# Performance work log

Hardware: AMD Instinct MI355X
Metric: run time of the kernel (lower is better)

## Reference

```python
import jax, jax.numpy as jnp
import numpy as np

N, C, T, V = 16, 64, 300, 25
NH, DK, DV = 4, 64, 64
DKH = DK // NH
DVH = DV // NH
EPS = 1e-5


def rel_to_abs(x):
    # x: (B, Nh, L, 2L-1) relative logits -> (B, Nh, L, L) absolute, via skew trick
    B, Nh, L, _ = x.shape
    x = jnp.pad(x, ((0, 0), (0, 0), (0, 0), (0, 1)))          # (B,Nh,L,2L)
    flat = x.reshape(B, Nh, L * 2 * L)
    flat = jnp.pad(flat, ((0, 0), (0, 0), (0, L - 1)))
    final = flat.reshape(B, Nh, L + 1, 2 * L - 1)
    return final[:, :, :L, L - 1:]


def setup_inputs() -> dict:
    key = jax.random.key(0)
    ks = jax.random.split(key, 12)
    return {
        "x": jax.random.normal(ks[0], (N, C, T, V), jnp.float32),
        "dbn_g": jax.random.normal(ks[1], (C * V,), jnp.float32),
        "dbn_b": jax.random.normal(ks[2], (C * V,), jnp.float32),
        "dbn_m": jax.random.normal(ks[3], (C * V,), jnp.float32) * 0.1,
        "dbn_v": jax.random.uniform(ks[4], (C * V,), jnp.float32, 0.5, 1.5),
        "qkv_w": jax.random.normal(ks[5], (2 * DK + DV, C), jnp.float32) * 0.05,
        "qkv_b": jax.random.normal(ks[6], (2 * DK + DV,), jnp.float32) * 0.05,
        "key_rel": jax.random.normal(ks[7], (2 * T - 1, DKH), jnp.float32),
        "attn_w": jax.random.normal(ks[8], (DV, DV), jnp.float32) * 0.05,
        "attn_b": jax.random.normal(ks[9], (DV,), jnp.float32) * 0.05,
        "bn_g": jax.random.normal(ks[10], (DV,), jnp.float32),
        "bn_b": jax.random.normal(ks[11], (DV,), jnp.float32),
        "bn_m": jnp.zeros((DV,), jnp.float32),
        "bn_v": jnp.ones((DV,), jnp.float32),
    }


def reference(x, dbn_g, dbn_b, dbn_m, dbn_v, qkv_w, qkv_b, key_rel,
              attn_w, attn_b, bn_g, bn_b, bn_m, bn_v):
    x_sum = x  # (N,C,T,V)
    # data_bn: BatchNorm1d (eval) over C*V channels on (N, C*V, T)
    xp = x.transpose(0, 1, 3, 2).reshape(N, C * V, T)
    xp = (xp - dbn_m[None, :, None]) * jax.lax.rsqrt(dbn_v + EPS)[None, :, None] \
         * dbn_g[None, :, None] + dbn_b[None, :, None]
    xn = xp.reshape(N, C, V, T).transpose(0, 1, 3, 2)          # (N,C,T,V)
    # per-joint temporal sequences: (N*V, C, T)
    xa = xn.transpose(0, 3, 1, 2).reshape(N * V, C, T)
    # 1x1 qkv conv
    qkv = jnp.einsum('oc,bct->bot', qkv_w, xa) + qkv_b[None, :, None]
    B = N * V
    q = qkv[:, :DK].reshape(B, NH, DKH, T) * (DKH ** -0.5)
    k = qkv[:, DK:2 * DK].reshape(B, NH, DKH, T)
    v = qkv[:, 2 * DK:].reshape(B, NH, DVH, T)
    logits = jnp.einsum('bhdt,bhds->bhts', q, k)               # (B,NH,T,T)
    rel = jnp.einsum('bhdt,md->bhtm', q, key_rel)              # (B,NH,T,2T-1)
    logits = logits + rel_to_abs(rel)
    w = jax.nn.softmax(logits, axis=-1)
    attn = jnp.einsum('bhts,bhds->bhtd', w, v)                 # (B,NH,T,DVH)
    attn = attn.transpose(0, 1, 3, 2).reshape(B, DV, T)        # combine heads
    attn = jnp.einsum('od,bdt->bot', attn_w, attn) + attn_b[None, :, None]
    out = attn.reshape(N, V, DV, T).transpose(0, 2, 3, 1)      # (N,DV,T,V)
    res = out + x_sum                                          # skip (down is None)
    res = (res - bn_m[None, :, None, None]) * jax.lax.rsqrt(bn_v + EPS)[None, :, None, None] \
          * bn_g[None, :, None, None] + bn_b[None, :, None, None]
    return jax.nn.relu(res)
```

## Files before the change

kernel.cpp:

```cpp
#include <hip/hip_runtime.h>
#include <hip/hip_bf16.h>
#include <cstddef>

#define NN 16
#define CC 64
#define TT 300
#define VV 25
#define NHH 4
#define DKHH 16
#define BB (NN * VV)
#define EPS 1e-5f
#define LOG2E 1.4426950408889634f

#define WS_QK    0
#define WS_V     7680000
#define WS_AH    11571200
#define WS_REL   15462400
#define WS_AWF   15472896
#define WS_AOFF  15474944
#define WS_SCO   15475008
#define WS_WFRAG 15475072
#define WS_QB2   15481216
#define WS_SCSH  15481408

typedef __attribute__((ext_vector_type(8))) short short8;
typedef __attribute__((ext_vector_type(4))) float float4v;

union U8 { short8 v; unsigned int w[4]; };

__device__ __forceinline__ unsigned int pk2(float a, float b) {
#if __has_builtin(__builtin_amdgcn_cvt_pk_bf16_f32)
    typedef __attribute__((ext_vector_type(2))) __bf16 bf2;
    union { bf2 v; unsigned u; } c;
    c.v = __builtin_amdgcn_cvt_pk_bf16_f32(a, b);
    return c.u;
#else
    union { float f; unsigned u; } x, y;
    x.f = a; y.f = b;
    unsigned ua = x.u + 0x7FFFu + ((x.u >> 16) & 1u);
    unsigned ub = y.u + 0x7FFFu + ((y.u >> 16) & 1u);
    return (ua >> 16) | (ub & 0xFFFF0000u);
#endif
}

__device__ __forceinline__ float ex2(float x) {
#if __has_builtin(__builtin_amdgcn_exp2f)
    return __builtin_amdgcn_exp2f(x);
#else
    return exp2f(x);
#endif
}

__device__ __forceinline__ float rcpf_(float x) {
#if __has_builtin(__builtin_amdgcn_rcpf)
    return __builtin_amdgcn_rcpf(x);
#else
    return 1.f / x;
#endif
}

__global__ __launch_bounds__(256) void k_pre(
    const float* __restrict__ dbn_g, const float* __restrict__ dbn_b,
    const float* __restrict__ dbn_m, const float* __restrict__ dbn_v,
    const float* __restrict__ qkv_w, const float* __restrict__ qkv_b,
    const float* __restrict__ key_rel,
    const float* __restrict__ attn_w, const float* __restrict__ attn_b,
    const float* __restrict__ bn_g, const float* __restrict__ bn_b,
    const float* __restrict__ bn_m, const float* __restrict__ bn_v,
    unsigned* __restrict__ W)
{
    const int jid = blockIdx.x * 256 + threadIdx.x;
    if (jid < 2624) {
        const int k = jid >> 6, lane = jid & 63, col = lane & 15, quad = lane >> 4;
        const int mt = k - 1, m = mt * 16 + col;
        const bool ok = (quad < 2) && (mt >= 0) && (m < 2 * TT - 1);
        unsigned w[4];
        #pragma unroll
        for (int j2 = 0; j2 < 4; ++j2) {
            const int c = quad * 8 + 2 * j2;
            const float v0 = ok ? key_rel[m * 16 + c] : 0.f;
            const float v1 = ok ? key_rel[m * 16 + c + 1] : 0.f;
            w[j2] = pk2(v0, v1);
        }
        *(uint4*)&W[WS_REL + k * 256 + lane * 4] = make_uint4(w[0], w[1], w[2], w[3]);
    } else if (jid < 3136) {
        const int e = jid - 2624;
        const int ot = e >> 7, ch = (e >> 6) & 1, lane = e & 63;
        const int col = lane & 15, quad = lane >> 4;
        const int o = ot * 16 + col;
        const float sc = bn_g[o] * rsqrtf(bn_v[o] + EPS);
        unsigned w[4];
        #pragma unroll
        for (int j2 = 0; j2 < 4; ++j2) {
            const int c = ch * 32 + quad * 8 + 2 * j2;
            w[j2] = pk2(attn_w[o * 64 + c] * sc, attn_w[o * 64 + c + 1] * sc);
        }
        *(uint4*)&W[WS_AWF + (ot * 2 + ch) * 256 + lane * 4] = make_uint4(w[0], w[1], w[2], w[3]);
    } else if (jid < 3200) {
        const int o = jid - 3136;
        const float sc = bn_g[o] * rsqrtf(bn_v[o] + EPS);
        ((float*)(W + WS_AOFF))[o] = attn_b[o] * sc + bn_b[o] - bn_m[o] * sc;
    } else if (jid < 3264) {
        const int o = jid - 3200;
        ((float*)(W + WS_SCO))[o] = bn_g[o] * rsqrtf(bn_v[o] + EPS);
    } else if (jid < 4800) {
        const int e = jid - 3264;
        const int ot = e >> 7, ch = (e >> 6) & 1, lane = e & 63;
        const int col = lane & 15, quad = lane >> 4;
        const int o = ot * 16 + col;
        const float qs = (o < 64) ? 0.25f * LOG2E : 1.f;
        unsigned w[4];
        #pragma unroll
        for (int j2 = 0; j2 < 4; ++j2) {
            const int c = ch * 32 + quad * 8 + 2 * j2;
            w[j2] = pk2(qkv_w[o * 64 + c] * qs, qkv_w[o * 64 + c + 1] * qs);
        }
        *(uint4*)&W[WS_WFRAG + (ot * 2 + ch) * 256 + lane * 4] = make_uint4(w[0], w[1], w[2], w[3]);
    } else if (jid < 4992) {
        const int o = jid - 4800;
        ((float*)(W + WS_QB2))[o] = qkv_b[o] * ((o < 64) ? 0.25f * LOG2E : 1.f);
    } else if (jid < 6592) {
        const int e = jid - 4992;
        const float sc = dbn_g[e] * rsqrtf(dbn_v[e] + EPS);
        const float sh = dbn_b[e] - dbn_m[e] * sc;
        ((float2*)(W + WS_SCSH))[e] = make_float2(sc, sh);
    }
}

__global__ __launch_bounds__(512) void k_qkv(
        const float* __restrict__ x, unsigned* __restrict__ W)
{
    const int tt = blockIdx.x, n = blockIdx.y, t0 = tt * 16;
    const int tid = threadIdx.x;
    const unsigned* wfrag = W + WS_WFRAG;
    const float* qb2 = (const float*)(W + WS_QB2);
    unsigned* qk_p = W + WS_QK;
    unsigned* v_p  = W + WS_V;

    __shared__ unsigned afrag[25 * 516];
    __shared__ float2 sls[1600];

    for (int i = tid; i < 1600; i += 512)
        sls[i] = ((const float2*)(W + WS_SCSH))[i];
    __syncthreads();

    for (int i = tid; i < 3200; i += 512) {
        const int f4 = i % 100, cp = i / 100;
        const int c0 = cp * 2;
        float4 xa = make_float4(0.f, 0.f, 0.f, 0.f);
        float4 xb = make_float4(0.f, 0.f, 0.f, 0.f);
        if (tt < 18 || f4 < 75) {
            const float* p = x + (size_t)(n * 64 + c0) * 7500 + tt * 400 + f4 * 4;
            xa = *(const float4*)p;
            xb = *(const float4*)(p + 7500);
        }
        const int ch = cp >> 4, qd = (cp >> 2) & 3, j2 = cp & 3;
        const float ea[4] = {xa.x, xa.y, xa.z, xa.w};
        const float eb[4] = {xb.x, xb.y, xb.z, xb.w};
        #pragma unroll
        for (int e = 0; e < 4; ++e) {
            const int flat = f4 * 4 + e;
            const int tl = (flat * 5243) >> 17;
            const int v  = flat - 25 * tl;
            const float2 s0 = sls[c0 * 25 + v];
            const float2 s1 = sls[c0 * 25 + 25 + v];
            const float a0 = fmaf(ea[e], s0.x, s0.y);
            const float a1 = fmaf(eb[e], s1.x, s1.y);
            afrag[v * 516 + (ch * 64 + qd * 16 + tl) * 4 + j2] = pk2(a0, a1);
        }
    }
    __syncthreads();

    const int wvv = tid >> 6, lane = tid & 63, col = lane & 15, quad = lane >> 4;
    const int otg = wvv >> 1, vh = wvv & 1;
    const int vlo = 13 * vh, vhi = vh ? 25 : 13;
    const float4v zero4 = {0.f, 0.f, 0.f, 0.f};
    const bool tvalid = (t0 + 4 * quad + 3 < TT);

    U8 bf[3][2]; float qb_l[3];
    #pragma unroll
    for (int i = 0; i < 3; ++i) {
        const int ot = 3 * otg + i;
        #pragma unroll
        for (int ch = 0; ch < 2; ++ch) {
            const uint4 u = *(const uint4*)&wfrag[(ot * 2 + ch) * 256 + lane * 4];
            bf[i][ch].w[0] = u.x; bf[i][ch].w[1] = u.y; bf[i][ch].w[2] = u.z; bf[i][ch].w[3] = u.w;
        }
        qb_l[i] = qb2[ot * 16 + col];
    }

    for (int v = vlo; v < vhi; ++v) {
        const int b = n * 25 + v;
        U8 a0, a1;
        { const uint4 u = *(const uint4*)&afrag[v * 516 + lane * 4];
          a0.w[0] = u.x; a0.w[1] = u.y; a0.w[2] = u.z; a0.w[3] = u.w; }
        { const uint4 u = *(const uint4*)&afrag[v * 516 + 256 + lane * 4];
          a1.w[0] = u.x; a1.w[1] = u.y; a1.w[2] = u.z; a1.w[3] = u.w; }
        #pragma unroll
        for (int i = 0; i < 3; ++i) {
            const int ot = 3 * otg + i;
            float4v acc = __builtin_amdgcn_mfma_f32_16x16x32_bf16(a0.v, bf[i][0].v, zero4, 0, 0, 0);
            acc = __builtin_amdgcn_mfma_f32_16x16x32_bf16(a1.v, bf[i][1].v, acc, 0, 0, 0);
            float val[4];
            #pragma unroll
            for (int r = 0; r < 4; ++r) val[r] = acc[r] + qb_l[i];
            if (ot < 8) {
                unsigned pk[4];
                #pragma unroll
                for (int r = 0; r < 4; ++r) {
                    const float p = __shfl_xor(val[r], 1);
                    pk[r] = pk2(val[r], p);
                }
                if (((col & 1) == 0) && tvalid) {
                    const int op = ot * 8 + (col >> 1);
                    *(uint4*)&qk_p[(size_t)(b * 64 + op) * TT + t0 + 4 * quad] =
                        make_uint4(pk[0], pk[1], pk[2], pk[3]);
                }
            } else {
                const int d = (ot - 8) * 16 + col;
                uint2 u;
                if (tvalid) { u.x = pk2(val[0], val[1]); u.y = pk2(val[2], val[3]); }
                else        { u.x = 0u; u.y = 0u; }
                *(uint2*)&v_p[(size_t)(b * 64 + d) * 152 + 8 * tt + 2 * quad] = u;
            }
        }
    }
}

__global__ __launch_bounds__(256, 4) void k_attn(unsigned* __restrict__ W)
{
    const int bh = blockIdx.x;
    const int half = blockIdx.y;
    const int b = bh >> 2, h = bh & 3;
    const int tid  = threadIdx.x;
    const int wave = tid >> 6, lane = tid & 63;
    const int col  = lane & 15, quad = lane >> 4;

    const unsigned* qk_p = W + WS_QK;
    const unsigned* v_p  = W + WS_V;
    unsigned* ah_p = W + WS_AH;
    const unsigned* relfrag = W + WS_REL;

    __shared__ unsigned kbuf[19 * 32 * 4];
    __shared__ unsigned vbuf[10 * 64 * 4];
    __shared__ float relbuf[4][16 * 68];

    for (int p = tid; p < 2432; p += 256) {
        const int c = p & 15, j2 = (p >> 4) & 3, qh = (p >> 6) & 1, st = p >> 7;
        kbuf[(st * 32 + qh * 16 + c) * 4 + j2] =
            qk_p[(size_t)(b * 64 + 32 + h * 8 + qh * 4 + j2) * TT + st * 16 + c];
    }
    for (int p = tid; p < 640; p += 256) {
        const int tq = p % 40, d = p / 40;
        const int off = (tq * 4 <= 148) ? tq * 4 : 144;
        const uint4 u = *(const uint4*)&v_p[(size_t)(b * 64 + h * 16 + d) * 152 + off];
        const int c = tq >> 2;
        const int l0 = (tq & 3) * 4;
        const unsigned uu[4] = {u.x, u.y, u.z, u.w};
        #pragma unroll
        for (int j = 0; j < 4; ++j) {
            const int local = l0 + j;
            const int q  = (local < 8) ? (local >> 1) : ((local - 8) >> 1);
            const int j2 = (local < 8) ? (local & 1) : (2 + (local & 1));
            vbuf[(c * 64 + q * 16 + d) * 4 + j2] = uu[j];
        }
    }
    __syncthreads();

    float* relw = &relbuf[wave][0];
    const float4v zero4 = {0.f, 0.f, 0.f, 0.f};
    U8 onef;
    onef.w[0] = onef.w[1] = onef.w[2] = onef.w[3] = 0x3F803F80u;

    const int ttlo = half ? 10 : 0;
    const int tthi = half ? 19 : 10;

    for (int tt = ttlo + wave; tt < tthi; tt += 4) {
        const int t0 = tt * 16;

        U8 qf;
        if (quad < 2) {
            int t = t0 + col; if (t > TT - 1) t = TT - 1;
            const size_t rb = (size_t)(b * 64 + h * 8 + quad * 4) * TT + t;
            qf.w[0] = qk_p[rb];
            qf.w[1] = qk_p[rb + TT];
            qf.w[2] = qk_p[rb + 2 * TT];
            qf.w[3] = qk_p[rb + 3 * TT];
        } else {
            qf.w[0] = qf.w[1] = qf.w[2] = qf.w[3] = 0u;
        }

        auto rel_ld = [&](int mt) -> uint4 {
            return *(const uint4*)&relfrag[(mt + 1) * 256 + lane * 4];
        };
        auto rel_do = [&](int mt, uint4 u) {
            U8 kr; kr.w[0] = u.x; kr.w[1] = u.y; kr.w[2] = u.z; kr.w[3] = u.w;
            const float4v rc = __builtin_amdgcn_mfma_f32_16x16x32_bf16(
                                   kr.v, qf.v, zero4, 0, 0, 0);
            const int wbase = mt * 16 + 4 * quad + t0 + col + 21;
            float* rw = &relw[col * 68];
            rw[wbase & 63]       = rc[0];
            rw[(wbase + 1) & 63] = rc[1];
            rw[(wbase + 2) & 63] = rc[2];
            rw[(wbase + 3) & 63] = rc[3];
        };

        #pragma unroll
        for (int i = 0; i < 4; ++i) rel_do(17 - tt + i, rel_ld(17 - tt + i));
        uint4 ru0 = rel_ld(21 - tt), ru1 = rel_ld(22 - tt);

        float4v accPV = zero4;
        float4v accS  = zero4;

        #pragma unroll 3
        for (int c = 0; c < 9; ++c) {
            U8 kf0, kf1;
            if (quad < 2) {
                const uint4 u0 = *(const uint4*)&kbuf[((2 * c) * 32 + quad * 16 + col) * 4];
                const uint4 u1 = *(const uint4*)&kbuf[((2 * c + 1) * 32 + quad * 16 + col) * 4];
                kf0.w[0] = u0.x; kf0.w[1] = u0.y; kf0.w[2] = u0.z; kf0.w[3] = u0.w;
                kf1.w[0] = u1.x; kf1.w[1] = u1.y; kf1.w[2] = u1.z; kf1.w[3] = u1.w;
            } else {
                kf0.w[0] = kf0.w[1] = kf0.w[2] = kf0.w[3] = 0u;
                kf1.w[0] = kf1.w[1] = kf1.w[2] = kf1.w[3] = 0u;
            }
            const short8 vf = *(const short8*)&vbuf[(c * 64 + lane) * 4];

            const int rb0 = (32 * c + 4 * quad) & 63;
            const float4v rc0 = *(const float4v*)&relw[col * 68 + rb0];
            const float4v rc1 = *(const float4v*)&relw[col * 68 + ((rb0 + 16) & 63)];
            const float4v qk0 = __builtin_amdgcn_mfma_f32_16x16x32_bf16(kf0.v, qf.v, rc0, 0, 0, 0);
            const float4v qk1 = __builtin_amdgcn_mfma_f32_16x16x32_bf16(kf1.v, qf.v, rc1, 0, 0, 0);

            const float e0 = ex2(qk0[0]);
            const float e1 = ex2(qk0[1]);
            const float e2 = ex2(qk0[2]);
            const float e3 = ex2(qk0[3]);
            const float e4 = ex2(qk1[0]);
            const float e5 = ex2(qk1[1]);
            const float e6 = ex2(qk1[2]);
            const float e7 = ex2(qk1[3]);

            U8 pf;
            pf.w[0] = pk2(e0, e1);
            pf.w[1] = pk2(e2, e3);
            pf.w[2] = pk2(e4, e5);
            pf.w[3] = pk2(e6, e7);
            accPV = __builtin_amdgcn_mfma_f32_16x16x32_bf16(pf.v, vf, accPV, 0, 0, 0);
            accS  = __builtin_amdgcn_mfma_f32_16x16x32_bf16(pf.v, onef.v, accS, 0, 0, 0);

            rel_do(2 * c + 21 - tt, ru0);
            rel_do(2 * c + 22 - tt, ru1);
            if (c < 8) { ru0 = rel_ld(2 * c + 23 - tt); ru1 = rel_ld(2 * c + 24 - tt); }
        }

        {
            U8 kf0;
            if (quad < 2) {
                const uint4 u0 = *(const uint4*)&kbuf[(18 * 32 + quad * 16 + col) * 4];
                kf0.w[0] = u0.x; kf0.w[1] = u0.y; kf0.w[2] = u0.z; kf0.w[3] = u0.w;
            } else {
                kf0.w[0] = kf0.w[1] = kf0.w[2] = kf0.w[3] = 0u;
            }
            const int rb0 = (288 + 4 * quad) & 63;
            const float4v rc0 = *(const float4v*)&relw[col * 68 + rb0];
            const float4v qk0 = __builtin_amdgcn_mfma_f32_16x16x32_bf16(kf0.v, qf.v, rc0, 0, 0, 0);
            float e0 = ex2(qk0[0]);
            float e1 = ex2(qk0[1]);
            float e2 = ex2(qk0[2]);
            float e3 = ex2(qk0[3]);
            if (quad == 3) { e0 = e1 = e2 = e3 = 0.f; }
            U8 pf;
            pf.w[0] = pk2(e0, e1);
            pf.w[1] = pk2(e2, e3);
            pf.w[2] = 0u;
            pf.w[3] = 0u;
            const short8 vf = *(const short8*)&vbuf[(9 * 64 + lane) * 4];
            accPV = __builtin_amdgcn_mfma_f32_16x16x32_bf16(pf.v, vf, accPV, 0, 0, 0);
            accS  = __builtin_amdgcn_mfma_f32_16x16x32_bf16(pf.v, onef.v, accS, 0, 0, 0);
        }

        if (t0 + 4 * quad + 3 < TT) {
            uint2 u;
            u.x = pk2(accPV[0] * rcpf_(accS[0]), accPV[1] * rcpf_(accS[1]));
            u.y = pk2(accPV[2] * rcpf_(accS[2]), accPV[3] * rcpf_(accS[3]));
            *(uint2*)&ah_p[(size_t)(b * 64 + h * 16 + col) * 152 + 8 * tt + 2 * quad] = u;
        }
    }
}

__global__ __launch_bounds__(512) void k_out(
        const float* __restrict__ x, const unsigned* __restrict__ W,
        float* __restrict__ out)
{
    const int tt = blockIdx.x, n = blockIdx.y, tq = blockIdx.z;
    if (tt == 18 && tq == 3) return;
    const int t0q = tt * 16 + tq * 4;
    const int tid = threadIdx.x;
    const unsigned* ah_p = W + WS_AH;
    const unsigned* awfrag = W + WS_AWF;
    const float* aoff = (const float*)(W + WS_AOFF);
    const float* scO  = (const float*)(W + WS_SCO);

    __shared__ unsigned fbuf[4 * 1024];
    __shared__ float obuf[6400];

    for (int j = tid; j < 1600; j += 512) {
        const int o = j / 25, f4 = j - 25 * o;
        const float4 xv = *(const float4*)(x + (size_t)(n * 64 + o) * 7500 + t0q * 25 + f4 * 4);
        *(float4*)&obuf[o * 100 + f4 * 4] = xv;
    }
    for (int i = tid; i < 1600; i += 512) {
        const int tp2 = i & 1, pc = (i >> 1) & 31, v = i >> 6;
        const int b = n * 25 + v;
        const size_t r0 = (size_t)(b * 64 + 2 * pc) * 152 + tt * 8 + tq * 2 + tp2;
        const unsigned A = ah_p[r0], Bv = ah_p[r0 + 152];
        const unsigned ue = (A & 0xFFFFu) | (Bv << 16);
        const unsigned uo = (A >> 16) | (Bv & 0xFFFF0000u);
        const int vt = v >> 4, cv = v & 15, ch = pc >> 4, qd = (pc >> 2) & 3, j2 = pc & 3;
        const int xi = (vt * 2 + ch) * 256 + (qd * 16 + (cv ^ qd)) * 4 + j2;
        const int tl = 2 * tp2;
        fbuf[tl * 1024 + ((xi + 12 * tl) & 1023)]             = ue;
        fbuf[(tl + 1) * 1024 + ((xi + 12 * (tl + 1)) & 1023)] = uo;
    }
    __syncthreads();

    const int wv = tid >> 6, lane = tid & 63, col = lane & 15, quad = lane >> 4;
    const int ow = wv & 3, th = wv >> 2;
    const int o = ow * 16 + col;
    const float4v zero4 = {0.f, 0.f, 0.f, 0.f};

    U8 awf0, awf1;
    { const uint4 u = *(const uint4*)&awfrag[(ow * 2 + 0) * 256 + lane * 4];
      awf0.w[0] = u.x; awf0.w[1] = u.y; awf0.w[2] = u.z; awf0.w[3] = u.w; }
    { const uint4 u = *(const uint4*)&awfrag[(ow * 2 + 1) * 256 + lane * 4];
      awf1.w[0] = u.x; awf1.w[1] = u.y; awf1.w[2] = u.z; awf1.w[3] = u.w; }
    const float aoff_l = aoff[o], sc_l = scO[o];

    for (int tl = 2 * th; tl < 2 * th + 2; ++tl) {
        #pragma unroll
        for (int vt = 0; vt < 2; ++vt) {
            U8 a0, a1;
            { const int xb = (vt * 2 + 0) * 256 + (quad * 16 + (col ^ quad)) * 4;
              const uint4 u = *(const uint4*)&fbuf[tl * 1024 + ((xb + 12 * tl) & 1023)];
              a0.w[0] = u.x; a0.w[1] = u.y; a0.w[2] = u.z; a0.w[3] = u.w; }
            { const int xb = (vt * 2 + 1) * 256 + (quad * 16 + (col ^ quad)) * 4;
              const uint4 u = *(const uint4*)&fbuf[tl * 1024 + ((xb + 12 * tl) & 1023)];
              a1.w[0] = u.x; a1.w[1] = u.y; a1.w[2] = u.z; a1.w[3] = u.w; }
            float4v acc = __builtin_amdgcn_mfma_f32_16x16x32_bf16(a0.v, awf0.v, zero4, 0, 0, 0);
            acc = __builtin_amdgcn_mfma_f32_16x16x32_bf16(a1.v, awf1.v, acc, 0, 0, 0);
            #pragma unroll
            for (int r = 0; r < 4; ++r) {
                const int v = vt * 16 + 4 * quad + r;
                if (v < 25) {
                    const int oi = o * 100 + tl * 25 + v;
                    obuf[oi] = fmaxf(fmaf(obuf[oi], sc_l, acc[r] + aoff_l), 0.f);
                }
            }
        }
    }
    __syncthreads();

    for (int j = tid; j < 1600; j += 512) {
        const int o2 = j / 25, f4 = j - 25 * o2;
        *(float4*)(out + (size_t)(n * 64 + o2) * 7500 + t0q * 25 + f4 * 4) =
            *(const float4*)&obuf[o2 * 100 + f4 * 4];
    }
}

extern "C" void kernel_launch(void* const* d_in, const int* in_sizes, int n_in,
                              void* d_out, int out_size, void* d_ws, size_t ws_size,
                              hipStream_t stream)
{
    const float* x       = (const float*)d_in[0];
    const float* dbn_g   = (const float*)d_in[1];
    const float* dbn_b   = (const float*)d_in[2];
    const float* dbn_m   = (const float*)d_in[3];
    const float* dbn_v   = (const float*)d_in[4];
    const float* qkv_w   = (const float*)d_in[5];
    const float* qkv_b   = (const float*)d_in[6];
    const float* key_rel = (const float*)d_in[7];
    const float* attn_w  = (const float*)d_in[8];
    const float* attn_b  = (const float*)d_in[9];
    const float* bn_g    = (const float*)d_in[10];
    const float* bn_b    = (const float*)d_in[11];
    const float* bn_m    = (const float*)d_in[12];
    const float* bn_v    = (const float*)d_in[13];
    float* out = (float*)d_out;
    unsigned* W = (unsigned*)d_ws;

    k_pre<<<26, 256, 0, stream>>>(dbn_g, dbn_b, dbn_m, dbn_v, qkv_w, qkv_b,
                                  key_rel, attn_w, attn_b, bn_g, bn_b, bn_m,
                                  bn_v, W);
    k_qkv<<<dim3(19, 16), 512, 0, stream>>>(x, W);
    k_attn<<<dim3(1600, 2), 256, 0, stream>>>(W);
    k_out<<<dim3(19, 16, 4), 512, 0, stream>>>(x, W, out);
}
```

Baseline: 233.8 us.

## Store V in MFMA fragment layout globally and read directly in attention

The QKV projection kernel now writes V straight into the per-(batch,head) MFMA B-fragment layout in global workspace, so the attention kernel drops its shared-memory V staging and the shuffle loop and loads fragments from global/L2 directly. Workspace offsets are shifted to fit the larger V region. The relative-logit scatter into the ring buffer is also simplified to contiguous stores with wrap handling only near the end. This saves LDS and prologue work, at the cost of uncached-in-LDS global reads of V inside the inner loop, repeated by both halves and every wave.

```diff
diff --git a/kernel.cpp b/kernel.cpp
--- a/kernel.cpp
+++ b/kernel.cpp
@@ -14,14 +14,14 @@
 
 #define WS_QK    0
 #define WS_V     7680000
-#define WS_AH    11571200
-#define WS_REL   15462400
-#define WS_AWF   15472896
-#define WS_AOFF  15474944
-#define WS_SCO   15475008
-#define WS_WFRAG 15475072
-#define WS_QB2   15481216
-#define WS_SCSH  15481408
+#define WS_AH    11776000
+#define WS_REL   15667200
+#define WS_AWF   15677696
+#define WS_AOFF  15679744
+#define WS_SCO   15679808
+#define WS_WFRAG 15679872
+#define WS_QB2   15686016
+#define WS_SCSH  15686208
 
 typedef __attribute__((ext_vector_type(8))) short short8;
 typedef __attribute__((ext_vector_type(4))) float float4v;
@@ -217,11 +217,26 @@
                         make_uint4(pk[0], pk[1], pk[2], pk[3]);
                 }
             } else {
-                const int d = (ot - 8) * 16 + col;
-                uint2 u;
-                if (tvalid) { u.x = pk2(val[0], val[1]); u.y = pk2(val[2], val[3]); }
-                else        { u.x = 0u; u.y = 0u; }
-                *(uint2*)&v_p[(size_t)(b * 64 + d) * 152 + 8 * tt + 2 * quad] = u;
+                const int hh = ot - 8, dd = col;
+                unsigned* vdst = v_p + (size_t)(b * 4 + hh) * 2560;
+                const unsigned ux = tvalid ? pk2(val[0], val[1]) : 0u;
+                const unsigned uy = tvalid ? pk2(val[2], val[3]) : 0u;
+                const int tp0 = 8 * tt + 2 * quad;
+                #pragma unroll
+                for (int e = 0; e < 2; ++e) {
+                    const int tp = tp0 + e;
+                    const int c9 = tp >> 4, l = tp & 15;
+                    const int qs = (l < 8) ? (l >> 1) : ((l - 8) >> 1);
+                    const int js = (l < 8) ? (l & 1) : (2 + (l & 1));
+                    vdst[(c9 * 64 + qs * 16 + dd) * 4 + js] = e ? uy : ux;
+                }
+                if (tt == 18 && quad == 3) {
+                    #pragma unroll
+                    for (int q = 0; q < 4; ++q) {
+                        vdst[(9 * 64 + q * 16 + dd) * 4 + 2] = 0u;
+                        vdst[(9 * 64 + q * 16 + dd) * 4 + 3] = 0u;
+                    }
+                }
             }
         }
     }
@@ -237,33 +252,17 @@
     const int col  = lane & 15, quad = lane >> 4;
 
     const unsigned* qk_p = W + WS_QK;
-    const unsigned* v_p  = W + WS_V;
+    const unsigned* vp   = W + WS_V + (size_t)(b * 4 + h) * 2560;
     unsigned* ah_p = W + WS_AH;
     const unsigned* relfrag = W + WS_REL;
 
     __shared__ unsigned kbuf[19 * 32 * 4];
-    __shared__ unsigned vbuf[10 * 64 * 4];
     __shared__ float relbuf[4][16 * 68];
 
     for (int p = tid; p < 2432; p += 256) {
         const int c = p & 15, j2 = (p >> 4) & 3, qh = (p >> 6) & 1, st = p >> 7;
         kbuf[(st * 32 + qh * 16 + c) * 4 + j2] =
             qk_p[(size_t)(b * 64 + 32 + h * 8 + qh * 4 + j2) * TT + st * 16 + c];
-    }
-    for (int p = tid; p < 640; p += 256) {
-        const int tq = p % 40, d = p / 40;
-        const int off = (tq * 4 <= 148) ? tq * 4 : 144;
-        const uint4 u = *(const uint4*)&v_p[(size_t)(b * 64 + h * 16 + d) * 152 + off];
-        const int c = tq >> 2;
-        const int l0 = (tq & 3) * 4;
-        const unsigned uu[4] = {u.x, u.y, u.z, u.w};
-        #pragma unroll
-        for (int j = 0; j < 4; ++j) {
-            const int local = l0 + j;
-            const int q  = (local < 8) ? (local >> 1) : ((local - 8) >> 1);
-            const int j2 = (local < 8) ? (local & 1) : (2 + (local & 1));
-            vbuf[(c * 64 + q * 16 + d) * 4 + j2] = uu[j];
-        }
     }
     __syncthreads();
 
@@ -297,12 +296,14 @@
             U8 kr; kr.w[0] = u.x; kr.w[1] = u.y; kr.w[2] = u.z; kr.w[3] = u.w;
             const float4v rc = __builtin_amdgcn_mfma_f32_16x16x32_bf16(
                                    kr.v, qf.v, zero4, 0, 0, 0);
-            const int wbase = mt * 16 + 4 * quad + t0 + col + 21;
-            float* rw = &relw[col * 68];
-            rw[wbase & 63]       = rc[0];
-            rw[(wbase + 1) & 63] = rc[1];
-            rw[(wbase + 2) & 63] = rc[2];
-            rw[(wbase + 3) & 63] = rc[3];
+            const int wb = (mt * 16 + 4 * quad + t0 + col + 21) & 63;
+            float* rw = &relw[col * 68 + wb];
+            rw[0] = rc[0]; rw[1] = rc[1]; rw[2] = rc[2]; rw[3] = rc[3];
+            if (wb > 60) {
+                #pragma unroll
+                for (int j = 1; j < 4; ++j)
+                    if (wb + j >= 64) relw[col * 68 + wb + j - 64] = rc[j];
+            }
         };
 
         #pragma unroll
@@ -324,7 +325,7 @@
                 kf0.w[0] = kf0.w[1] = kf0.w[2] = kf0.w[3] = 0u;
                 kf1.w[0] = kf1.w[1] = kf1.w[2] = kf1.w[3] = 0u;
             }
-            const short8 vf = *(const short8*)&vbuf[(c * 64 + lane) * 4];
+            const short8 vf = *(const short8*)&vp[(c * 64 + lane) * 4];
 
             const int rb0 = (32 * c + 4 * quad) & 63;
             const float4v rc0 = *(const float4v*)&relw[col * 68 + rb0];
@@ -375,7 +376,7 @@
             pf.w[1] = pk2(e2, e3);
             pf.w[2] = 0u;
             pf.w[3] = 0u;
-            const short8 vf = *(const short8*)&vbuf[(9 * 64 + lane) * 4];
+            const short8 vf = *(const short8*)&vp[(9 * 64 + lane) * 4];
             accPV = __builtin_amdgcn_mfma_f32_16x16x32_bf16(pf.v, vf, accPV, 0, 0, 0);
             accS  = __builtin_amdgcn_mfma_f32_16x16x32_bf16(pf.v, onef.v, accS, 0, 0, 0);
         }
```

New measurement: 243.5 us. +4.2%, slower.
